# Optimization experiments

Measured on AMD Instinct MI355X. Metric: run time of the kernel, lower is better.

Reference implementation:

```python
import jax, jax.numpy as jnp
import numpy as np

EPS = 1e-4      # MovingBatchNorm eps
STEPS = 3       # fixed RK4 steps standing in for adaptive dopri5
B, N, D, C, H = 4, 2048, 3, 64, 512


def setup_inputs() -> dict:
    key = jax.random.key(0)
    ks = iter(jax.random.split(key, 40))
    f32 = jnp.float32

    def rn(shape, s=1.0):
        return jax.random.normal(next(ks), shape, dtype=f32) * s

    inp = {}
    inp['x'] = rn((B, N, D))
    inp['c'] = rn((B, N, C))
    for p in ('bn1', 'bn2'):
        inp[p + '_mean'] = rn((D,), 0.1)
        inp[p + '_var'] = jax.random.uniform(next(ks), (D,), dtype=f32, minval=0.5, maxval=1.5)
        inp[p + '_log_gamma'] = jnp.zeros((D,), f32)
        inp[p + '_beta'] = jnp.zeros((D,), f32)
    inp['sqrt_T'] = jnp.array([np.sqrt(0.5)], f32)  # train_T: T = sqrt_T**2
    dims = [(D, H), (H, H), (H, H), (H, D)]  # concatsquash (in, out)
    for i, (din, dout) in enumerate(dims):
        inp[f'W{i}'] = rn((dout, din), 0.05)
        inp[f'b{i}'] = jnp.zeros((dout,), f32)
        inp[f'Wg{i}'] = rn((dout, C + 1), 0.05)
        inp[f'bg{i}'] = jnp.zeros((dout,), f32)
        inp[f'Wb{i}'] = rn((dout, C + 1), 0.05)
    return inp


def _odenet(t, x, c, layers):
    # ConcatSquash MLP: lin(x)*sigmoid(hyper_gate([t,c])) + hyper_bias([t,c])
    ctx = jnp.concatenate([jnp.broadcast_to(t, c.shape[:-1] + (1,)).astype(x.dtype), c], axis=-1)
    h = x
    for i, (W, b, Wg, bg, Wb) in enumerate(layers):
        h = (h @ W.T + b) * jax.nn.sigmoid(ctx @ Wg.T + bg) + ctx @ Wb.T
        if i < len(layers) - 1:
            h = jnp.tanh(h)
    return h


def _aug_dyn(t, x, c, layers):
    # augmented CNF dynamics: (dx/dt, dlogp/dt) with exact divergence via D jvps
    f = lambda xx: _odenet(t, xx, c, layers)
    div = jnp.zeros(x.shape[:-1] + (1,), x.dtype)
    dx = None
    for i in range(x.shape[-1]):
        e = jnp.zeros_like(x).at[..., i].set(1.0)
        dx, jv = jax.jvp(f, (x,), (e,))
        div = div + jv[..., i:i + 1]
    return dx, -div


def _rk4(x0, lp0, c, layers, T):
    dt = T / STEPS

    def step(carry, i):
        x, lp = carry
        t = i.astype(x.dtype) * dt
        k1x, k1l = _aug_dyn(t, x, c, layers)
        k2x, k2l = _aug_dyn(t + 0.5 * dt, x + 0.5 * dt * k1x, c, layers)
        k3x, k3l = _aug_dyn(t + 0.5 * dt, x + 0.5 * dt * k2x, c, layers)
        k4x, k4l = _aug_dyn(t + dt, x + dt * k3x, c, layers)
        x = x + (dt / 6.0) * (k1x + 2.0 * k2x + 2.0 * k3x + k4x)
        lp = lp + (dt / 6.0) * (k1l + 2.0 * k2l + 2.0 * k3l + k4l)
        return (x, lp), None

    (x, lp), _ = jax.lax.scan(step, (x0, lp0), jnp.arange(STEPS))
    return x, lp


def _bn(x, lp, mean, var, log_gamma, beta):
    # MovingBatchNorm1d, eval mode; logdet = sum(log_gamma - 0.5*log(var+eps))
    y = (x - mean) * jnp.exp(log_gamma) / jnp.sqrt(var + EPS) + beta
    ld = jnp.sum(log_gamma - 0.5 * jnp.log(var + EPS))
    return y, lp - ld


def reference(x, c, bn1_mean, bn1_var, bn1_log_gamma, bn1_beta,
              bn2_mean, bn2_var, bn2_log_gamma, bn2_beta, sqrt_T,
              W0, b0, Wg0, bg0, Wb0, W1, b1, Wg1, bg1, Wb1,
              W2, b2, Wg2, bg2, Wb2, W3, b3, Wg3, bg3, Wb3):
    layers = [(W0, b0, Wg0, bg0, Wb0), (W1, b1, Wg1, bg1, Wb1),
              (W2, b2, Wg2, bg2, Wb2), (W3, b3, Wg3, bg3, Wb3)]
    lp = jnp.zeros(x.shape[:-1] + (1,), x.dtype)  # (B,N,1)
    x, lp = _bn(x, lp, bn1_mean, bn1_var, bn1_log_gamma, bn1_beta)
    T = sqrt_T[0] ** 2
    x, lp = _rk4(x, lp, c, layers, T)
    x, lp = _bn(x, lp, bn2_mean, bn2_var, bn2_log_gamma, bn2_beta)
    return x, jnp.sum(lp, axis=(1, 2))
```

## Files before the change

kernel.cpp:

```cpp
#include <hip/hip_runtime.h>
#include <hip/hip_fp8.h>

#define PTS 8192
#define HDIM 512
#define BN_EPS 1e-4f
#define HSTRB 528
#define TS 256.0f
#define SCL1 0x7f7f7f7f

typedef unsigned short u16;
typedef unsigned char u8;
typedef long long i64;
typedef u16 u16x8 __attribute__((ext_vector_type(8)));
typedef short s16x8 __attribute__((ext_vector_type(8)));
typedef float f32x4 __attribute__((ext_vector_type(4)));
typedef float f32x2 __attribute__((ext_vector_type(2)));
typedef int i32x4 __attribute__((ext_vector_type(4)));
typedef int i32x8 __attribute__((ext_vector_type(8)));

__device__ __forceinline__ float bf2f(u16 u) {
  unsigned x = ((unsigned)u) << 16;
  return __builtin_bit_cast(float, x);
}
__device__ __forceinline__ u16 f2bf(float f) {
  unsigned x = __builtin_bit_cast(unsigned, f);
  x += 0x7fffu + ((x >> 16) & 1u);
  return (u16)(x >> 16);
}
__device__ __forceinline__ u8 f2f8(float x) {
  int v = __builtin_amdgcn_cvt_pk_fp8_f32(x, x, 0, false);
  return (u8)(v & 0xff);
}
__device__ __forceinline__ unsigned pk4_f8(float a, float b, float c, float d) {
  int v = __builtin_amdgcn_cvt_pk_fp8_f32(a, b, 0, false);
  v = __builtin_amdgcn_cvt_pk_fp8_f32(c, d, v, true);
  return (unsigned)v;
}
__device__ __forceinline__ float sigf(float x) {
  return __builtin_amdgcn_rcpf(1.f + __expf(-x));
}
__device__ __forceinline__ float fast_tanh(float x) {
  float e = __expf(2.f * x);
  return 1.f - 2.f * __builtin_amdgcn_rcpf(e + 1.f);
}
__device__ __forceinline__ void gl2lds16(const u16* g, u16* l) {
  __builtin_amdgcn_global_load_lds(
      (const __attribute__((address_space(1))) void*)g,
      (__attribute__((address_space(3))) void*)l, 16, 0, 0);
}
__device__ __forceinline__ i32x8 ld32(const u8* p) {
  i32x4 lo = *(const i32x4*)p;
  i32x4 hi = *(const i32x4*)(p + 16);
  return __builtin_shufflevector(lo, hi, 0, 1, 2, 3, 4, 5, 6, 7);
}

#define MFMA_SC(A, B, C) \
  __builtin_amdgcn_mfma_scale_f32_16x16x128_f8f6f4((A), (B), (C), 0, 0, 0, SCL1, 0, SCL1)

#define MX_HALF(WL, HB, H)                                                  \
  {                                                                         \
    _Pragma("unroll")                                                       \
    for (int zi = 0; zi < 2; ++zi)                                          \
      _Pragma("unroll")                                                     \
      for (int zj = 0; zj < 2; ++zj)                                        \
        _Pragma("unroll")                                                   \
        for (int zr = 0; zr < 4; ++zr) acc[zi][zj][zr] = 0.f;               \
    const u8* wp = (WL) + (H) * 4096;                                       \
    _Pragma("unroll 1")                                                     \
    for (int c = 0; c < 4; ++c) {                                           \
      const u8* hc = (HB) + c * 128;                                        \
      i32x8 af0 = ld32(hc);                                                 \
      i32x8 af1 = ld32(hc + (size_t)16 * HSTRB);                            \
      i32x8 bA = ld32(wp);                                                  \
      i32x8 bB = ld32(wp + 2048);                                           \
      __builtin_amdgcn_sched_barrier(0);                                    \
      __builtin_amdgcn_s_setprio(1);                                        \
      acc[0][0] = MFMA_SC(af0, bA, acc[0][0]);                              \
      acc[1][0] = MFMA_SC(af1, bA, acc[1][0]);                              \
      acc[0][1] = MFMA_SC(af0, bB, acc[0][1]);                              \
      acc[1][1] = MFMA_SC(af1, bB, acc[1][1]);                              \
      __builtin_amdgcn_s_setprio(0);                                        \
      __builtin_amdgcn_sched_barrier(0);                                    \
      wp += 65536;                                                          \
    }                                                                       \
  }

#define EPI1_HALF(H)                                                        \
  {                                                                         \
    asm("" : "+v"(g1p));                                                    \
    unsigned g1v[2][2];                                                     \
    _Pragma("unroll")                                                       \
    for (int jl = 0; jl < 2; ++jl)                                          \
      _Pragma("unroll")                                                     \
      for (int i = 0; i < 2; ++i)                                           \
        g1v[jl][i] = *(const unsigned*)(g1p + (size_t)i * 4096 +            \
                                        ((H) * 2 + jl) * 32);               \
    _Pragma("unroll")                                                       \
    for (int jl = 0; jl < 2; ++jl) {                                        \
      int n = n0 + ((H) * 2 + jl) * 16 + lr;                                \
      f32x4 e1 = *(const f32x4*)(a.E1 + (size_t)n * 4);                     \
      _Pragma("unroll")                                                     \
      for (int i = 0; i < 2; ++i) {                                         \
        unsigned d = g1v[jl][i];                                            \
        float gate = sigf(bf2f((u16)(d & 0xffffu)) + t * e1[1]);            \
        float bias = bf2f((u16)(d >> 16)) + t * e1[2];                      \
        f32x4 u = acc[i][jl];                                               \
        float z = fmaf(u[0] + e1[0], gate, bias);                           \
        float hh = fast_tanh(z);                                            \
        float wmf = (1.f - hh * hh) * gate;                                 \
        int row = i * 16 + quad * 4;                                        \
        HsB[(size_t)row * HSTRB + n] = f2f8(hh);                            \
        HsB[(size_t)(row + 1) * HSTRB + n] = f2f8(u[1] * wmf);              \
        HsB[(size_t)(row + 2) * HSTRB + n] = f2f8(u[2] * wmf);              \
        HsB[(size_t)(row + 3) * HSTRB + n] = f2f8(u[3] * wmf);              \
      }                                                                     \
    }                                                                       \
  }

#define EPI2_HALF(H)                                                        \
  {                                                                         \
    asm("" : "+v"(g2p));                                                    \
    unsigned g2v[2][2];                                                     \
    _Pragma("unroll")                                                       \
    for (int jl = 0; jl < 2; ++jl)                                          \
      _Pragma("unroll")                                                     \
      for (int i = 0; i < 2; ++i)                                           \
        g2v[jl][i] = *(const unsigned*)(g2p + (size_t)i * 4096 +            \
                                        ((H) * 2 + jl) * 32);               \
    _Pragma("unroll")                                                       \
    for (int i = 0; i < 2; ++i) {                                           \
      float v0 = 0.f, v1 = 0.f, v2 = 0.f, v3 = 0.f, v4 = 0.f, v5 = 0.f;     \
      _Pragma("unroll")                                                     \
      for (int jl = 0; jl < 2; ++jl) {                                      \
        int n = n0 + ((H) * 2 + jl) * 16 + lr;                              \
        f32x4 ea = *(const f32x4*)(a.E2 + (size_t)n * 8);                   \
        f32x2 eb = *(const f32x2*)(a.E2 + (size_t)n * 8 + 4);               \
        unsigned d = g2v[jl][i];                                            \
        float gate = sigf(bf2f((u16)(d & 0xffffu)) + t * ea[1]);            \
        float bias = bf2f((u16)(d >> 16)) + t * ea[2];                      \
        f32x4 u = acc[i][jl];                                               \
        float z = fmaf(u[0] + ea[0], gate, bias);                           \
        float hh = fast_tanh(z);                                            \
        float wmf = (1.f - hh * hh) * gate;                                 \
        float w30 = ea[3], w31 = eb[0], w32 = eb[1];                        \
        v0 = fmaf(hh, w30, v0);                                             \
        v1 = fmaf(hh, w31, v1);                                             \
        v2 = fmaf(hh, w32, v2);                                             \
        v3 = fmaf(u[1] * wmf, w30, v3);                                     \
        v4 = fmaf(u[2] * wmf, w31, v4);                                     \
        v5 = fmaf(u[3] * wmf, w32, v5);                                     \
      }                                                                     \
      _Pragma("unroll")                                                     \
      for (int mask = 1; mask <= 8; mask <<= 1) {                           \
        v0 += __shfl_xor(v0, mask);                                         \
        v1 += __shfl_xor(v1, mask);                                         \
        v2 += __shfl_xor(v2, mask);                                         \
        v3 += __shfl_xor(v3, mask);                                         \
        v4 += __shfl_xor(v4, mask);                                         \
        v5 += __shfl_xor(v5, mask);                                         \
      }                                                                     \
      float val = (lr == 0) ? v0 : (lr == 1) ? v1 : (lr == 2) ? v2          \
                : (lr == 3) ? v3 * (1.f / TS) : (lr == 4) ? v4 * (1.f / TS) \
                : v5 * (1.f / TS);                                          \
      int pl = i * 4 + quad;                                                \
      if (lr < 6) {                                                         \
        if ((H) == 0) part[w][pl][lr] = val;                                \
        else part[w][pl][lr] += val;                                        \
      }                                                                     \
    }                                                                       \
  }

struct PrepArgs {
  const float *W1, *W2;
  u8 *W1s, *W2s;
  const float* c;
  u16* cb;
  const float *Wg0, *Wg1, *Wg2, *Wb0, *Wb1, *Wb2;
  const float *bg0, *bg1, *bg2;
  u16* Wpack;
  float* bias_pack;
  const float *x, *m1, *v1, *lg1, *be1;
  float *x_cur;
  const float *Wg3, *bg3, *Wb3;
  float *G3, *B3;
  const float *W0, *b0, *b1, *b2, *W3;
  float *E0, *E1, *E2;
};
__global__ void prep_kernel(PrepArgs a) {
  int i = blockIdx.x * 256 + threadIdx.x;
  if (i < 512 * 512) {
    int n = i >> 9, k = i & 511;
    int c = k >> 7, q2 = (k >> 5) & 3, b = k & 31;
    int w = n >> 6, j = (n >> 4) & 3, lr = n & 15;
    size_t d = (size_t)c * 65536 + (size_t)w * 8192 + (size_t)j * 2048 +
               (size_t)(q2 * 16 + lr) * 32 + b;
    a.W1s[d] = f2f8(a.W1[i]);
    a.W2s[d] = f2f8(a.W2[i]);
  }
  if (i < PTS * 64) a.cb[i] = f2bf(a.c[i]);
  if (i < 6 * 512 * 64) {
    int sec = i >> 15;
    int within = i & 32767;
    int o = within >> 6, k = within & 63;
    const float* src[6] = {a.Wg0, a.Wg1, a.Wg2, a.Wb0, a.Wb1, a.Wb2};
    a.Wpack[i] = f2bf(src[sec][o * 65 + 1 + k]);
  }
  if (i < 3072) {
    int sec = i >> 9, o = i & 511;
    const float* bgl[3] = {a.bg0, a.bg1, a.bg2};
    a.bias_pack[i] = (sec < 3) ? bgl[sec][o] : 0.f;
  }
  if (i < 512) {
    int o = i;
    a.E0[o * 8 + 0] = a.W0[o * 3];
    a.E0[o * 8 + 1] = a.W0[o * 3 + 1];
    a.E0[o * 8 + 2] = a.W0[o * 3 + 2];
    a.E0[o * 8 + 3] = a.b0[o];
    a.E0[o * 8 + 4] = a.Wg0[o * 65];
    a.E0[o * 8 + 5] = a.Wb0[o * 65];
    a.E0[o * 8 + 6] = 0.f; a.E0[o * 8 + 7] = 0.f;
    a.E1[o * 4 + 0] = a.b1[o];
    a.E1[o * 4 + 1] = a.Wg1[o * 65];
    a.E1[o * 4 + 2] = a.Wb1[o * 65];
    a.E1[o * 4 + 3] = 0.f;
    a.E2[o * 8 + 0] = a.b2[o];
    a.E2[o * 8 + 1] = a.Wg2[o * 65];
    a.E2[o * 8 + 2] = a.Wb2[o * 65];
    a.E2[o * 8 + 3] = a.W3[o];
    a.E2[o * 8 + 4] = a.W3[512 + o];
    a.E2[o * 8 + 5] = a.W3[1024 + o];
    a.E2[o * 8 + 6] = 0.f; a.E2[o * 8 + 7] = 0.f;
  }
  if (i < PTS * 3) {
    int d = i % 3;
    a.x_cur[i] = (a.x[i] - a.m1[d]) * __expf(a.lg1[d]) * rsqrtf(a.v1[d] + BN_EPS) + a.be1[d];
  }
  {
    int lane = threadIdx.x & 63;
    int p = (blockIdx.x * 256 + threadIdx.x) >> 6;
    float cv = a.c[(size_t)p * 64 + lane];
    float ag[3], ab[3];
    #pragma unroll
    for (int o = 0; o < 3; ++o) {
      ag[o] = cv * a.Wg3[o * 65 + 1 + lane];
      ab[o] = cv * a.Wb3[o * 65 + 1 + lane];
    }
    #pragma unroll
    for (int off = 32; off > 0; off >>= 1) {
      #pragma unroll
      for (int o = 0; o < 3; ++o) {
        ag[o] += __shfl_xor(ag[o], off);
        ab[o] += __shfl_xor(ab[o], off);
      }
    }
    if (lane == 0) {
      #pragma unroll
      for (int o = 0; o < 3; ++o) {
        a.G3[p * 3 + o] = ag[o] + a.bg3[o];
        a.B3[p * 3 + o] = ab[o];
      }
    }
  }
}

struct GatesGemmArgs {
  const u16 *A, *W;
  const float* bias;
  u16* GBi;
};
__global__ __launch_bounds__(256) void gates_gemm(GatesGemmArgs a) {
  __shared__ u16 As[128 * 32];
  __shared__ u16 Bs[128 * 32];
  int tid = threadIdx.x;
  int m0 = blockIdx.x * 128, n0 = blockIdx.y * 128;
  int wave = tid >> 6, lane = tid & 63;
  int wm = (wave & 1) * 64, wn = (wave >> 1) * 64;
  int lr = lane & 15, quad = lane >> 4;

  int rowS = tid >> 2, colS = (tid & 3) * 8;
  const u16* gA0 = a.A + (size_t)(m0 + rowS) * 64 + colS;
  const u16* gB0 = a.W + (size_t)(n0 + rowS) * 64 + colS;
  u16* sA0 = &As[tid * 8];
  u16* sA1 = &As[2048 + tid * 8];
  u16* sB0 = &Bs[tid * 8];
  u16* sB1 = &Bs[2048 + tid * 8];

  f32x4 acc[4][4];
  #pragma unroll
  for (int i = 0; i < 4; ++i)
    #pragma unroll
    for (int j = 0; j < 4; ++j)
      #pragma unroll
      for (int r = 0; r < 4; ++r) acc[i][j][r] = 0.f;

  for (int k0 = 0; k0 < 64; k0 += 32) {
    if (k0) __syncthreads();
    gl2lds16(gA0 + k0, sA0);
    gl2lds16(gA0 + (size_t)64 * 64 + k0, sA1);
    gl2lds16(gB0 + k0, sB0);
    gl2lds16(gB0 + (size_t)64 * 64 + k0, sB1);
    __syncthreads();
    s16x8 af[4], bfr[4];
    #pragma unroll
    for (int i = 0; i < 4; ++i)
      af[i] = *(const s16x8*)&As[(wm + i * 16 + lr) * 32 + quad * 8];
    #pragma unroll
    for (int j = 0; j < 4; ++j)
      bfr[j] = *(const s16x8*)&Bs[(wn + j * 16 + lr) * 32 + quad * 8];
    #pragma unroll
    for (int i = 0; i < 4; ++i)
      #pragma unroll
      for (int j = 0; j < 4; ++j)
        acc[i][j] = __builtin_amdgcn_mfma_f32_16x16x32_bf16(af[i], bfr[j], acc[i][j], 0, 0, 0);
  }

  #pragma unroll
  for (int j = 0; j < 4; ++j) {
    int n = n0 + wn + j * 16 + lr;
    int sec = n >> 9, col = n & 511;
    int l = (sec < 3) ? sec : sec - 3;
    int off = col * 2 + ((sec < 3) ? 0 : 1);
    float bv = a.bias[n];
    u16* outp = a.GBi + (size_t)l * PTS * 1024 + off;
    #pragma unroll
    for (int i = 0; i < 4; ++i) {
      int mrow = m0 + wm + i * 16 + quad * 4;
      #pragma unroll
      for (int r = 0; r < 4; ++r)
        outp[(size_t)(mrow + r) * 1024] = f2bf(acc[i][j][r] + bv);
    }
  }
}

struct FlowArgs {
  const float* sqrtT;
  const float *G3, *B3, *Wg3, *Wb3, *b3;
  const float* x0;
  const u16 *GBi0, *GBi1, *GBi2;
  const float *E0, *E1, *E2;
  const u8 *W1s, *W2s;
  const float *m2, *v2, *lg2, *be2;
  float* out_x;
  float* lp_state;
};

__global__ __launch_bounds__(512, 6) void flow_kernel(FlowArgs a) {
  __shared__ __align__(16) u8 HsA[32 * HSTRB];
  __shared__ __align__(16) u8 HsB[32 * HSTRB];
  __shared__ float part[8][8][8];
  __shared__ float xs[2][8][3], kxs[8][3];
  __shared__ float kls[8], lps[8];
  __shared__ float g3s[8][3], b3s[8][3];

  int tid = threadIdx.x;
  int w = tid >> 6, lane = tid & 63, lr = lane & 15, quad = lane >> 4;
  int n0 = w * 64;
  int p0 = blockIdx.x * 8;
  int pl0 = tid >> 6;
  int base_o = (tid & 63) * 8;
  bool desig = (tid & 63) == 0;
  float s0 = a.sqrtT[0];
  float dt = s0 * s0 * (1.f / 3.f);

  const u8* w1l = a.W1s + (size_t)w * 8192 + (size_t)lane * 32;
  const u8* w2l = a.W2s + (size_t)w * 8192 + (size_t)lane * 32;
  const u8* hbA = (const u8*)HsA + (size_t)lr * HSTRB + quad * 32;
  const u8* hbB = (const u8*)HsB + (size_t)lr * HSTRB + quad * 32;

  float wg3r[3], wb3r[3], b3r[3];
  #pragma unroll
  for (int r = 0; r < 3; ++r) {
    wg3r[r] = a.Wg3[r * 65];
    wb3r[r] = a.Wb3[r * 65];
    b3r[r] = a.b3[r];
  }

  const u16* g0p = a.GBi0 + (size_t)(p0 + pl0) * 1024 + 2 * base_o;
  const u16* g1p = a.GBi1 + (size_t)(p0 + quad) * 1024 + 2 * (n0 + lr);
  const u16* g2p = a.GBi2 + (size_t)(p0 + quad) * 1024 + 2 * (n0 + lr);

  if (desig) {
    #pragma unroll
    for (int r = 0; r < 3; ++r) {
      xs[0][pl0][r] = a.x0[(p0 + pl0) * 3 + r];
      g3s[pl0][r] = a.G3[(p0 + pl0) * 3 + r];
      b3s[pl0][r] = a.B3[(p0 + pl0) * 3 + r];
    }
    lps[pl0] = 0.f;
  }
  u16x8 gc0 = *(const u16x8*)(g0p);
  u16x8 gc1 = *(const u16x8*)(g0p + 8);
  __syncthreads();

  #pragma unroll 1
  for (int s = 0; s < 12; ++s) {
    int sub = s & 3;
    float t = ((float)(s >> 2) + ((sub == 0) ? 0.f : (sub == 3) ? 1.f : 0.5f)) * dt;

    float o0, o1, o2;
    if (s == 0) {
      o0 = xs[0][pl0][0]; o1 = xs[0][pl0][1]; o2 = xs[0][pl0][2];
    } else {
      int m = (s - 1) & 3, q = (s - 1) >> 2;
      float tp = ((float)q + ((m == 0) ? 0.f : (m == 3) ? 1.f : 0.5f)) * dt;
      float fr0 = 0.f, fr1 = 0.f, fr2 = 0.f, fr3 = 0.f, fr4 = 0.f, fr5 = 0.f;
      #pragma unroll
      for (int ww = 0; ww < 8; ++ww) {
        f32x4 pa = *(const f32x4*)&part[ww][pl0][0];
        f32x2 pb = *(const f32x2*)&part[ww][pl0][4];
        fr0 += pa[0]; fr1 += pa[1]; fr2 += pa[2];
        fr3 += pa[3]; fr4 += pb[0]; fr5 += pb[1];
      }
      float ga0 = sigf(g3s[pl0][0] + tp * wg3r[0]);
      float ga1 = sigf(g3s[pl0][1] + tp * wg3r[1]);
      float ga2 = sigf(g3s[pl0][2] + tp * wg3r[2]);
      float dx0 = fmaf(fr0 + b3r[0], ga0, b3s[pl0][0] + tp * wb3r[0]);
      float dx1 = fmaf(fr1 + b3r[1], ga1, b3s[pl0][1] + tp * wb3r[1]);
      float dx2 = fmaf(fr2 + b3r[2], ga2, b3s[pl0][2] + tp * wb3r[2]);
      float klv = -(fr3 * ga0 + fr4 * ga1 + fr5 * ga2);
      float bx0 = xs[q & 1][pl0][0];
      float bx1 = xs[q & 1][pl0][1];
      float bx2 = xs[q & 1][pl0][2];
      if (m == 3) {
        float sc = dt * (1.f / 6.f);
        o0 = bx0 + sc * (kxs[pl0][0] + dx0);
        o1 = bx1 + sc * (kxs[pl0][1] + dx1);
        o2 = bx2 + sc * (kxs[pl0][2] + dx2);
        if (desig) {
          xs[(q + 1) & 1][pl0][0] = o0;
          xs[(q + 1) & 1][pl0][1] = o1;
          xs[(q + 1) & 1][pl0][2] = o2;
          lps[pl0] += sc * (kls[pl0] + klv);
        }
      } else {
        float cf = (m == 2) ? dt : 0.5f * dt;
        o0 = fmaf(cf, dx0, bx0);
        o1 = fmaf(cf, dx1, bx1);
        o2 = fmaf(cf, dx2, bx2);
        if (desig) {
          if (m == 0) {
            kxs[pl0][0] = dx0; kxs[pl0][1] = dx1; kxs[pl0][2] = dx2;
            kls[pl0] = klv;
          } else {
            kxs[pl0][0] += 2.f * dx0; kxs[pl0][1] += 2.f * dx1; kxs[pl0][2] += 2.f * dx2;
            kls[pl0] += 2.f * klv;
          }
        }
      }
    }

    {
      u16x8 gcv[2] = {gc0, gc1};
      #pragma unroll
      for (int cc = 0; cc < 2; ++cc) {
        u16x8 v = gcv[cc];
        float hk[4], d0k[4], d1k[4], d2k[4];
        #pragma unroll
        for (int k = 0; k < 4; ++k) {
          int o = base_o + cc * 4 + k;
          f32x4 e = *(const f32x4*)(a.E0 + (size_t)o * 8);
          f32x2 e2 = *(const f32x2*)(a.E0 + (size_t)o * 8 + 4);
          float u = fmaf(e[0], o0, fmaf(e[1], o1, e[2] * o2)) + e[3];
          float gate = sigf(bf2f(v[2 * k]) + t * e2[0]);
          float bias = bf2f(v[2 * k + 1]) + t * e2[1];
          float z = fmaf(u, gate, bias);
          float h = fast_tanh(z);
          float wm = (1.f - h * h) * gate * TS;
          hk[k] = h;
          d0k[k] = wm * e[0];
          d1k[k] = wm * e[1];
          d2k[k] = wm * e[2];
        }
        size_t hbb = (size_t)(pl0 * 4) * HSTRB + base_o + cc * 4;
        *(unsigned*)(HsA + hbb) = pk4_f8(hk[0], hk[1], hk[2], hk[3]);
        *(unsigned*)(HsA + hbb + HSTRB) = pk4_f8(d0k[0], d0k[1], d0k[2], d0k[3]);
        *(unsigned*)(HsA + hbb + 2 * HSTRB) = pk4_f8(d1k[0], d1k[1], d1k[2], d1k[3]);
        *(unsigned*)(HsA + hbb + 3 * HSTRB) = pk4_f8(d2k[0], d2k[1], d2k[2], d2k[3]);
      }
    }
    __syncthreads();

    f32x4 acc[2][2];
    MX_HALF(w1l, hbA, 0)
    EPI1_HALF(0)
    MX_HALF(w1l, hbA, 1)
    EPI1_HALF(1)
    __syncthreads();

    MX_HALF(w2l, hbB, 0)
    EPI2_HALF(0)
    MX_HALF(w2l, hbB, 1)
    asm("" : "+v"(g0p));
    gc0 = *(const u16x8*)(g0p);
    gc1 = *(const u16x8*)(g0p + 8);
    EPI2_HALF(1)
    __syncthreads();
  }

  if (desig) {
    int p = p0 + pl0;
    float tp = 3.f * dt;
    float fr0 = 0.f, fr1 = 0.f, fr2 = 0.f, fr3 = 0.f, fr4 = 0.f, fr5 = 0.f;
    #pragma unroll
    for (int ww = 0; ww < 8; ++ww) {
      f32x4 pa = *(const f32x4*)&part[ww][pl0][0];
      f32x2 pb = *(const f32x2*)&part[ww][pl0][4];
      fr0 += pa[0]; fr1 += pa[1]; fr2 += pa[2];
      fr3 += pa[3]; fr4 += pb[0]; fr5 += pb[1];
    }
    float ga0 = sigf(g3s[pl0][0] + tp * wg3r[0]);
    float ga1 = sigf(g3s[pl0][1] + tp * wg3r[1]);
    float ga2 = sigf(g3s[pl0][2] + tp * wg3r[2]);
    float dx[3];
    dx[0] = fmaf(fr0 + b3r[0], ga0, b3s[pl0][0] + tp * wb3r[0]);
    dx[1] = fmaf(fr1 + b3r[1], ga1, b3s[pl0][1] + tp * wb3r[1]);
    dx[2] = fmaf(fr2 + b3r[2], ga2, b3s[pl0][2] + tp * wb3r[2]);
    float klv = -(fr3 * ga0 + fr4 * ga1 + fr5 * ga2);
    float sc = dt * (1.f / 6.f);
    #pragma unroll
    for (int r = 0; r < 3; ++r) {
      float xf = xs[0][pl0][r] + sc * (kxs[pl0][r] + dx[r]);
      a.out_x[p * 3 + r] =
          (xf - a.m2[r]) * __expf(a.lg2[r]) * rsqrtf(a.v2[r] + BN_EPS) + a.be2[r];
    }
    a.lp_state[p] = lps[pl0] + sc * (kls[pl0] + klv);
  }
}

__global__ void finish_lp(const float* __restrict__ lp_state,
                          const float* __restrict__ v1, const float* __restrict__ lg1,
                          const float* __restrict__ v2, const float* __restrict__ lg2,
                          float* __restrict__ out) {
  int b = blockIdx.x, tid = threadIdx.x;
  float s = 0.f;
  for (int n = tid; n < 2048; n += 256) s += lp_state[b * 2048 + n];
  __shared__ float red[256];
  red[tid] = s;
  __syncthreads();
  for (int w = 128; w > 0; w >>= 1) {
    if (tid < w) red[tid] += red[tid + w];
    __syncthreads();
  }
  if (tid == 0) {
    float ld = 0.f;
    for (int d = 0; d < 3; ++d) {
      ld += lg1[d] - 0.5f * logf(v1[d] + BN_EPS);
      ld += lg2[d] - 0.5f * logf(v2[d] + BN_EPS);
    }
    out[b] = red[0] - 2048.f * ld;
  }
}

extern "C" void kernel_launch(void* const* d_in, const int* in_sizes, int n_in,
                              void* d_out, int out_size, void* d_ws, size_t ws_size,
                              hipStream_t stream) {
  const float* x        = (const float*)d_in[0];
  const float* c        = (const float*)d_in[1];
  const float* bn1_mean = (const float*)d_in[2];
  const float* bn1_var  = (const float*)d_in[3];
  const float* bn1_lg   = (const float*)d_in[4];
  const float* bn1_beta = (const float*)d_in[5];
  const float* bn2_mean = (const float*)d_in[6];
  const float* bn2_var  = (const float*)d_in[7];
  const float* bn2_lg   = (const float*)d_in[8];
  const float* bn2_beta = (const float*)d_in[9];
  const float* sqrtT    = (const float*)d_in[10];
  const float* W0  = (const float*)d_in[11];
  const float* b0  = (const float*)d_in[12];
  const float* Wg0 = (const float*)d_in[13];
  const float* bg0 = (const float*)d_in[14];
  const float* Wb0 = (const float*)d_in[15];
  const float* W1  = (const float*)d_in[16];
  const float* b1  = (const float*)d_in[17];
  const float* Wg1 = (const float*)d_in[18];
  const float* bg1 = (const float*)d_in[19];
  const float* Wb1 = (const float*)d_in[20];
  const float* W2  = (const float*)d_in[21];
  const float* b2  = (const float*)d_in[22];
  const float* Wg2 = (const float*)d_in[23];
  const float* bg2 = (const float*)d_in[24];
  const float* Wb2 = (const float*)d_in[25];
  const float* W3  = (const float*)d_in[26];
  const float* b3  = (const float*)d_in[27];
  const float* Wg3 = (const float*)d_in[28];
  const float* bg3 = (const float*)d_in[29];
  const float* Wb3 = (const float*)d_in[30];

  char* base = (char*)d_ws;
  size_t off = 0;
  auto alloc = [&](size_t bytes) -> void* {
    void* pp = base + off;
    off += (bytes + 255) & ~(size_t)255;
    return pp;
  };
  u8* W1s = (u8*)alloc((size_t)512 * 512);
  u8* W2s = (u8*)alloc((size_t)512 * 512);
  u16* cb  = (u16*)alloc((size_t)PTS * 64 * 2);
  u16* Wpack = (u16*)alloc((size_t)6 * 512 * 64 * 2);
  float* bias_pack = (float*)alloc((size_t)3072 * 4);
  u16* GBi = (u16*)alloc((size_t)3 * PTS * 1024 * 2);
  const size_t SZi = (size_t)PTS * 1024;
  u16* GBi0 = GBi;
  u16* GBi1 = GBi + SZi;
  u16* GBi2 = GBi + 2 * SZi;
  float* G3f = (float*)alloc((size_t)PTS * 3 * 4);
  float* B3f = (float*)alloc((size_t)PTS * 3 * 4);
  float* E0 = (float*)alloc((size_t)512 * 8 * 4);
  float* E1 = (float*)alloc((size_t)512 * 4 * 4);
  float* E2 = (float*)alloc((size_t)512 * 8 * 4);
  float* x_cur    = (float*)alloc((size_t)PTS * 3 * 4);
  float* lp_state = (float*)alloc((size_t)PTS * 4);
  (void)ws_size; (void)in_sizes; (void)n_in; (void)out_size;

  PrepArgs pa{W1, W2, W1s, W2s, c, cb, Wg0, Wg1, Wg2, Wb0, Wb1, Wb2,
              bg0, bg1, bg2, Wpack, bias_pack, x, bn1_mean, bn1_var,
              bn1_lg, bn1_beta, x_cur, Wg3, bg3, Wb3, G3f, B3f,
              W0, b0, b1, b2, W3, E0, E1, E2};
  prep_kernel<<<2048, 256, 0, stream>>>(pa);

  GatesGemmArgs gg{cb, Wpack, bias_pack, GBi};
  gates_gemm<<<dim3(64, 24), 256, 0, stream>>>(gg);

  FlowArgs fa{sqrtT, G3f, B3f, Wg3, Wb3, b3, x_cur, GBi0, GBi1, GBi2,
              E0, E1, E2, W1s, W2s, bn2_mean, bn2_var, bn2_lg, bn2_beta,
              (float*)d_out, lp_state};
  flow_kernel<<<PTS / 8, 512, 0, stream>>>(fa);

  finish_lp<<<4, 256, 0, stream>>>(lp_state, bn1_var, bn1_lg, bn2_var, bn2_lg,
                                   (float*)d_out + PTS * 3);
}
```

Before: 643.2 us.

## Process two point groups per block and interleave their layer pipelines

Each block now handles 16 points split into two 8-point halves with double-buffered activation tiles. The MFMA work of one half overlaps the epilogue and layer-0 work of the other. Each wave's GEMM tile widens to 4 column groups, so each A fragment load feeds twice as many MFMAs. This halves the grid and cuts per-block weight re-reads and barriers per point. The cost is higher register and LDS pressure and a more complex schedule.

After: 726.7 us. 1.13x slower.

```diff
diff --git a/kernel.cpp b/kernel.cpp
--- a/kernel.cpp
+++ b/kernel.cpp
@@ -57,117 +57,217 @@
 #define MFMA_SC(A, B, C) \
   __builtin_amdgcn_mfma_scale_f32_16x16x128_f8f6f4((A), (B), (C), 0, 0, 0, SCL1, 0, SCL1)
 
-#define MX_HALF(WL, HB, H)                                                  \
+#define MXCHUNK(ACC, WP, HC)                                                \
+    {                                                                       \
+      i32x8 af0 = ld32(HC);                                                 \
+      i32x8 af1 = ld32((HC) + (size_t)16 * HSTRB);                          \
+      i32x8 bA = ld32(WP);                                                  \
+      i32x8 bB = ld32((WP) + 2048);                                         \
+      __builtin_amdgcn_sched_barrier(0);                                    \
+      __builtin_amdgcn_s_setprio(1);                                        \
+      ACC[0][0] = MFMA_SC(af0, bA, ACC[0][0]);                              \
+      ACC[1][0] = MFMA_SC(af1, bA, ACC[1][0]);                              \
+      ACC[0][1] = MFMA_SC(af0, bB, ACC[0][1]);                              \
+      ACC[1][1] = MFMA_SC(af1, bB, ACC[1][1]);                              \
+      __builtin_amdgcn_s_setprio(0);                                        \
+      __builtin_amdgcn_sched_barrier(0);                                    \
+      bA = ld32((WP) + 4096);                                               \
+      bB = ld32((WP) + 6144);                                               \
+      __builtin_amdgcn_sched_barrier(0);                                    \
+      __builtin_amdgcn_s_setprio(1);                                        \
+      ACC[0][2] = MFMA_SC(af0, bA, ACC[0][2]);                              \
+      ACC[1][2] = MFMA_SC(af1, bA, ACC[1][2]);                              \
+      ACC[0][3] = MFMA_SC(af0, bB, ACC[0][3]);                              \
+      ACC[1][3] = MFMA_SC(af1, bB, ACC[1][3]);                              \
+      __builtin_amdgcn_s_setprio(0);                                        \
+      __builtin_amdgcn_sched_barrier(0);                                    \
+    }
+
+#define MXG(ACC, WL, HB, PREFETCH)                                          \
   {                                                                         \
     _Pragma("unroll")                                                       \
     for (int zi = 0; zi < 2; ++zi)                                          \
       _Pragma("unroll")                                                     \
-      for (int zj = 0; zj < 2; ++zj)                                        \
+      for (int zj = 0; zj < 4; ++zj)                                        \
         _Pragma("unroll")                                                   \
-        for (int zr = 0; zr < 4; ++zr) acc[zi][zj][zr] = 0.f;               \
-    const u8* wp = (WL) + (H) * 4096;                                       \
+        for (int zr = 0; zr < 4; ++zr) ACC[zi][zj][zr] = 0.f;               \
+    const u8* wp = (WL);                                                    \
     _Pragma("unroll 1")                                                     \
-    for (int c = 0; c < 4; ++c) {                                           \
+    for (int c = 0; c < 3; ++c) {                                           \
       const u8* hc = (HB) + c * 128;                                        \
-      i32x8 af0 = ld32(hc);                                                 \
-      i32x8 af1 = ld32(hc + (size_t)16 * HSTRB);                            \
-      i32x8 bA = ld32(wp);                                                  \
-      i32x8 bB = ld32(wp + 2048);                                           \
-      __builtin_amdgcn_sched_barrier(0);                                    \
-      __builtin_amdgcn_s_setprio(1);                                        \
-      acc[0][0] = MFMA_SC(af0, bA, acc[0][0]);                              \
-      acc[1][0] = MFMA_SC(af1, bA, acc[1][0]);                              \
-      acc[0][1] = MFMA_SC(af0, bB, acc[0][1]);                              \
-      acc[1][1] = MFMA_SC(af1, bB, acc[1][1]);                              \
-      __builtin_amdgcn_s_setprio(0);                                        \
-      __builtin_amdgcn_sched_barrier(0);                                    \
+      MXCHUNK(ACC, wp, hc)                                                  \
       wp += 65536;                                                          \
     }                                                                       \
-  }
-
-#define EPI1_HALF(H)                                                        \
+    PREFETCH                                                                \
+    {                                                                       \
+      const u8* hc = (HB) + 3 * 128;                                        \
+      MXCHUNK(ACC, wp, hc)                                                  \
+    }                                                                       \
+  }
+
+#define FOLDM(HH, SS)                                                       \
   {                                                                         \
-    asm("" : "+v"(g1p));                                                    \
-    unsigned g1v[2][2];                                                     \
+    int ptg = (HH) * 8 + ptl;                                               \
+    if ((SS) == 0) {                                                        \
+      o0 = xs[0][ptg][0]; o1 = xs[0][ptg][1]; o2 = xs[0][ptg][2];           \
+    } else {                                                                \
+      int m = ((SS) - 1) & 3, q = ((SS) - 1) >> 2;                          \
+      float tp = ((float)q + ((m == 0) ? 0.f : (m == 3) ? 1.f : 0.5f)) * dt;\
+      float fr0 = 0.f, fr1 = 0.f, fr2 = 0.f, fr3 = 0.f, fr4 = 0.f, fr5 = 0.f;\
+      _Pragma("unroll")                                                     \
+      for (int ww = 0; ww < 8; ++ww) {                                      \
+        f32x4 pa = *(const f32x4*)&part[ww][ptg][0];                        \
+        f32x2 pb = *(const f32x2*)&part[ww][ptg][4];                        \
+        fr0 += pa[0]; fr1 += pa[1]; fr2 += pa[2];                           \
+        fr3 += pa[3]; fr4 += pb[0]; fr5 += pb[1];                           \
+      }                                                                     \
+      float ga0 = sigf(g3s[ptg][0] + tp * a.Wg3[0]);                        \
+      float ga1 = sigf(g3s[ptg][1] + tp * a.Wg3[65]);                       \
+      float ga2 = sigf(g3s[ptg][2] + tp * a.Wg3[130]);                      \
+      float dx0 = fmaf(fr0 + a.b3[0], ga0, b3s[ptg][0] + tp * a.Wb3[0]);    \
+      float dx1 = fmaf(fr1 + a.b3[1], ga1, b3s[ptg][1] + tp * a.Wb3[65]);   \
+      float dx2 = fmaf(fr2 + a.b3[2], ga2, b3s[ptg][2] + tp * a.Wb3[130]);  \
+      float klv = -(fr3 * ga0 + fr4 * ga1 + fr5 * ga2);                     \
+      float bx0 = xs[q & 1][ptg][0];                                        \
+      float bx1 = xs[q & 1][ptg][1];                                        \
+      float bx2 = xs[q & 1][ptg][2];                                        \
+      if (m == 3) {                                                         \
+        float sc = dt * (1.f / 6.f);                                        \
+        o0 = bx0 + sc * (kxs[ptg][0] + dx0);                                \
+        o1 = bx1 + sc * (kxs[ptg][1] + dx1);                                \
+        o2 = bx2 + sc * (kxs[ptg][2] + dx2);                                \
+        if (desig) {                                                        \
+          xs[(q + 1) & 1][ptg][0] = o0;                                     \
+          xs[(q + 1) & 1][ptg][1] = o1;                                     \
+          xs[(q + 1) & 1][ptg][2] = o2;                                     \
+          lps[ptg] += sc * (kls[ptg] + klv);                                \
+        }                                                                   \
+      } else {                                                              \
+        float cf = (m == 2) ? dt : 0.5f * dt;                               \
+        o0 = fmaf(cf, dx0, bx0);                                            \
+        o1 = fmaf(cf, dx1, bx1);                                            \
+        o2 = fmaf(cf, dx2, bx2);                                            \
+        if (desig) {                                                        \
+          if (m == 0) {                                                     \
+            kxs[ptg][0] = dx0; kxs[ptg][1] = dx1; kxs[ptg][2] = dx2;        \
+            kls[ptg] = klv;                                                 \
+          } else {                                                          \
+            kxs[ptg][0] += 2.f * dx0; kxs[ptg][1] += 2.f * dx1;             \
+            kxs[ptg][2] += 2.f * dx2;                                       \
+            kls[ptg] += 2.f * klv;                                          \
+          }                                                                 \
+        }                                                                   \
+      }                                                                     \
+    }                                                                       \
+  }
+
+#define L0M(HD, TT)                                                         \
+  {                                                                         \
     _Pragma("unroll")                                                       \
-    for (int jl = 0; jl < 2; ++jl)                                          \
+    for (int cc = 0; cc < 2; ++cc) {                                        \
+      u16x8 v = cc ? gcB : gcA;                                             \
+      float hk[4], d0k[4], d1k[4], d2k[4];                                  \
+      _Pragma("unroll")                                                     \
+      for (int k = 0; k < 4; ++k) {                                         \
+        int o = colb + cc * 4 + k;                                          \
+        f32x4 e = *(const f32x4*)(a.E0 + (size_t)o * 8);                    \
+        f32x2 e2 = *(const f32x2*)(a.E0 + (size_t)o * 8 + 4);               \
+        float u = fmaf(e[0], o0, fmaf(e[1], o1, e[2] * o2)) + e[3];         \
+        float gate = sigf(bf2f(v[2 * k]) + (TT) * e2[0]);                   \
+        float bias = bf2f(v[2 * k + 1]) + (TT) * e2[1];                     \
+        float z = fmaf(u, gate, bias);                                      \
+        float hh = fast_tanh(z);                                            \
+        float wm = (1.f - hh * hh) * gate * TS;                             \
+        hk[k] = hh;                                                         \
+        d0k[k] = wm * e[0];                                                 \
+        d1k[k] = wm * e[1];                                                 \
+        d2k[k] = wm * e[2];                                                 \
+      }                                                                     \
+      size_t hbb = (size_t)(ptl * 4) * HSTRB + colb + cc * 4;               \
+      *(unsigned*)((HD) + hbb) = pk4_f8(hk[0], hk[1], hk[2], hk[3]);        \
+      *(unsigned*)((HD) + hbb + HSTRB) = pk4_f8(d0k[0], d0k[1], d0k[2], d0k[3]); \
+      *(unsigned*)((HD) + hbb + 2 * HSTRB) = pk4_f8(d1k[0], d1k[1], d1k[2], d1k[3]); \
+      *(unsigned*)((HD) + hbb + 3 * HSTRB) = pk4_f8(d2k[0], d2k[1], d2k[2], d2k[3]); \
+    }                                                                       \
+  }
+
+#define EPI1M(ACC, HD)                                                      \
+  _Pragma("unroll")                                                         \
+  for (int j = 0; j < 4; ++j) {                                             \
+    int n = n0 + j * 16 + lr;                                               \
+    f32x4 e1 = *(const f32x4*)(a.E1 + (size_t)n * 4);                       \
+    _Pragma("unroll")                                                       \
+    for (int i = 0; i < 2; ++i) {                                           \
+      unsigned d = gv[j][i];                                                \
+      float gate = sigf(bf2f((u16)(d & 0xffffu)) + t * e1[1]);              \
+      float bias = bf2f((u16)(d >> 16)) + t * e1[2];                        \
+      f32x4 u = ACC[i][j];                                                  \
+      float z = fmaf(u[0] + e1[0], gate, bias);                             \
+      float hh = fast_tanh(z);                                              \
+      float wmf = (1.f - hh * hh) * gate;                                   \
+      int row = i * 16 + quad * 4;                                          \
+      (HD)[(size_t)row * HSTRB + n] = f2f8(hh);                             \
+      (HD)[(size_t)(row + 1) * HSTRB + n] = f2f8(u[1] * wmf);               \
+      (HD)[(size_t)(row + 2) * HSTRB + n] = f2f8(u[2] * wmf);               \
+      (HD)[(size_t)(row + 3) * HSTRB + n] = f2f8(u[3] * wmf);               \
+    }                                                                       \
+  }
+
+#define EPI2M(ACC, HH)                                                      \
+  _Pragma("unroll")                                                         \
+  for (int i = 0; i < 2; ++i) {                                             \
+    float v0 = 0.f, v1 = 0.f, v2 = 0.f, v3 = 0.f, v4 = 0.f, v5 = 0.f;       \
+    _Pragma("unroll")                                                       \
+    for (int j = 0; j < 4; ++j) {                                           \
+      int n = n0 + j * 16 + lr;                                             \
+      f32x4 ea = *(const f32x4*)(a.E2 + (size_t)n * 8);                     \
+      f32x2 eb = *(const f32x2*)(a.E2 + (size_t)n * 8 + 4);                 \
+      unsigned d = gv[j][i];                                                \
+      float gate = sigf(bf2f((u16)(d & 0xffffu)) + t * ea[1]);              \
+      float bias = bf2f((u16)(d >> 16)) + t * ea[2];                        \
+      f32x4 u = ACC[i][j];                                                  \
+      float z = fmaf(u[0] + ea[0], gate, bias);                             \
+      float hh = fast_tanh(z);                                              \
+      float wmf = (1.f - hh * hh) * gate;                                   \
+      float w30 = ea[3], w31 = eb[0], w32 = eb[1];                          \
+      v0 = fmaf(hh, w30, v0);                                               \
+      v1 = fmaf(hh, w31, v1);                                               \
+      v2 = fmaf(hh, w32, v2);                                               \
+      v3 = fmaf(u[1] * wmf, w30, v3);                                       \
+      v4 = fmaf(u[2] * wmf, w31, v4);                                       \
+      v5 = fmaf(u[3] * wmf, w32, v5);                                       \
+    }                                                                       \
+    _Pragma("unroll")                                                       \
+    for (int mask = 1; mask <= 8; mask <<= 1) {                             \
+      v0 += __shfl_xor(v0, mask);                                           \
+      v1 += __shfl_xor(v1, mask);                                           \
+      v2 += __shfl_xor(v2, mask);                                           \
+      v3 += __shfl_xor(v3, mask);                                           \
+      v4 += __shfl_xor(v4, mask);                                           \
+      v5 += __shfl_xor(v5, mask);                                           \
+    }                                                                       \
+    float val = (lr == 0) ? v0 : (lr == 1) ? v1 : (lr == 2) ? v2            \
+              : (lr == 3) ? v3 * (1.f / TS) : (lr == 4) ? v4 * (1.f / TS)   \
+              : v5 * (1.f / TS);                                            \
+    if (lr < 6) part[w][(HH) * 8 + i * 4 + quad][lr] = val;                 \
+  }
+
+#define GLD(BP, HH)                                                         \
+  {                                                                         \
+    const u16* gp_ = (BP); asm("" : "+v"(gp_));                             \
+    _Pragma("unroll")                                                       \
+    for (int j = 0; j < 4; ++j)                                             \
       _Pragma("unroll")                                                     \
       for (int i = 0; i < 2; ++i)                                           \
-        g1v[jl][i] = *(const unsigned*)(g1p + (size_t)i * 4096 +            \
-                                        ((H) * 2 + jl) * 32);               \
-    _Pragma("unroll")                                                       \
-    for (int jl = 0; jl < 2; ++jl) {                                        \
-      int n = n0 + ((H) * 2 + jl) * 16 + lr;                                \
-      f32x4 e1 = *(const f32x4*)(a.E1 + (size_t)n * 4);                     \
-      _Pragma("unroll")                                                     \
-      for (int i = 0; i < 2; ++i) {                                         \
-        unsigned d = g1v[jl][i];                                            \
-        float gate = sigf(bf2f((u16)(d & 0xffffu)) + t * e1[1]);            \
-        float bias = bf2f((u16)(d >> 16)) + t * e1[2];                      \
-        f32x4 u = acc[i][jl];                                               \
-        float z = fmaf(u[0] + e1[0], gate, bias);                           \
-        float hh = fast_tanh(z);                                            \
-        float wmf = (1.f - hh * hh) * gate;                                 \
-        int row = i * 16 + quad * 4;                                        \
-        HsB[(size_t)row * HSTRB + n] = f2f8(hh);                            \
-        HsB[(size_t)(row + 1) * HSTRB + n] = f2f8(u[1] * wmf);              \
-        HsB[(size_t)(row + 2) * HSTRB + n] = f2f8(u[2] * wmf);              \
-        HsB[(size_t)(row + 3) * HSTRB + n] = f2f8(u[3] * wmf);              \
-      }                                                                     \
-    }                                                                       \
-  }
-
-#define EPI2_HALF(H)                                                        \
+        gv[j][i] = *(const unsigned*)(gp_ + (HH) * 8192 +                   \
+                                      (size_t)i * 4096 + j * 32);           \
+  }
+
+#define GCLD(HH)                                                            \
   {                                                                         \
-    asm("" : "+v"(g2p));                                                    \
-    unsigned g2v[2][2];                                                     \
-    _Pragma("unroll")                                                       \
-    for (int jl = 0; jl < 2; ++jl)                                          \
-      _Pragma("unroll")                                                     \
-      for (int i = 0; i < 2; ++i)                                           \
-        g2v[jl][i] = *(const unsigned*)(g2p + (size_t)i * 4096 +            \
-                                        ((H) * 2 + jl) * 32);               \
-    _Pragma("unroll")                                                       \
-    for (int i = 0; i < 2; ++i) {                                           \
-      float v0 = 0.f, v1 = 0.f, v2 = 0.f, v3 = 0.f, v4 = 0.f, v5 = 0.f;     \
-      _Pragma("unroll")                                                     \
-      for (int jl = 0; jl < 2; ++jl) {                                      \
-        int n = n0 + ((H) * 2 + jl) * 16 + lr;                              \
-        f32x4 ea = *(const f32x4*)(a.E2 + (size_t)n * 8);                   \
-        f32x2 eb = *(const f32x2*)(a.E2 + (size_t)n * 8 + 4);               \
-        unsigned d = g2v[jl][i];                                            \
-        float gate = sigf(bf2f((u16)(d & 0xffffu)) + t * ea[1]);            \
-        float bias = bf2f((u16)(d >> 16)) + t * ea[2];                      \
-        f32x4 u = acc[i][jl];                                               \
-        float z = fmaf(u[0] + ea[0], gate, bias);                           \
-        float hh = fast_tanh(z);                                            \
-        float wmf = (1.f - hh * hh) * gate;                                 \
-        float w30 = ea[3], w31 = eb[0], w32 = eb[1];                        \
-        v0 = fmaf(hh, w30, v0);                                             \
-        v1 = fmaf(hh, w31, v1);                                             \
-        v2 = fmaf(hh, w32, v2);                                             \
-        v3 = fmaf(u[1] * wmf, w30, v3);                                     \
-        v4 = fmaf(u[2] * wmf, w31, v4);                                     \
-        v5 = fmaf(u[3] * wmf, w32, v5);                                     \
-      }                                                                     \
-      _Pragma("unroll")                                                     \
-      for (int mask = 1; mask <= 8; mask <<= 1) {                           \
-        v0 += __shfl_xor(v0, mask);                                         \
-        v1 += __shfl_xor(v1, mask);                                         \
-        v2 += __shfl_xor(v2, mask);                                         \
-        v3 += __shfl_xor(v3, mask);                                         \
-        v4 += __shfl_xor(v4, mask);                                         \
-        v5 += __shfl_xor(v5, mask);                                         \
-      }                                                                     \
-      float val = (lr == 0) ? v0 : (lr == 1) ? v1 : (lr == 2) ? v2          \
-                : (lr == 3) ? v3 * (1.f / TS) : (lr == 4) ? v4 * (1.f / TS) \
-                : v5 * (1.f / TS);                                          \
-      int pl = i * 4 + quad;                                                \
-      if (lr < 6) {                                                         \
-        if ((H) == 0) part[w][pl][lr] = val;                                \
-        else part[w][pl][lr] += val;                                        \
-      }                                                                     \
-    }                                                                       \
+    const u16* gp_ = g0p + (HH) * 8192; asm("" : "+v"(gp_));                \
+    gcA = *(const u16x8*)(gp_);                                             \
+    gcB = *(const u16x8*)(gp_ + 8);                                         \
   }
 
 struct PrepArgs {
@@ -344,186 +444,120 @@
   float* lp_state;
 };
 
-__global__ __launch_bounds__(512, 6) void flow_kernel(FlowArgs a) {
-  __shared__ __align__(16) u8 HsA[32 * HSTRB];
-  __shared__ __align__(16) u8 HsB[32 * HSTRB];
-  __shared__ float part[8][8][8];
-  __shared__ float xs[2][8][3], kxs[8][3];
-  __shared__ float kls[8], lps[8];
-  __shared__ float g3s[8][3], b3s[8][3];
+__global__ __launch_bounds__(512, 4) void flow_kernel(FlowArgs a) {
+  __shared__ __align__(16) u8 HA0[32 * HSTRB];
+  __shared__ __align__(16) u8 HA1[32 * HSTRB];
+  __shared__ __align__(16) u8 HB0[32 * HSTRB];
+  __shared__ __align__(16) u8 HB1[32 * HSTRB];
+  __shared__ float part[8][16][8];
+  __shared__ float xs[2][16][3], kxs[16][3];
+  __shared__ float kls[16], lps[16];
+  __shared__ float g3s[16][3], b3s[16][3];
 
   int tid = threadIdx.x;
   int w = tid >> 6, lane = tid & 63, lr = lane & 15, quad = lane >> 4;
   int n0 = w * 64;
-  int p0 = blockIdx.x * 8;
-  int pl0 = tid >> 6;
-  int base_o = (tid & 63) * 8;
+  int p0 = blockIdx.x * 16;
+  int ptl = tid >> 6;
+  int colb = (tid & 63) * 8;
   bool desig = (tid & 63) == 0;
   float s0 = a.sqrtT[0];
   float dt = s0 * s0 * (1.f / 3.f);
 
   const u8* w1l = a.W1s + (size_t)w * 8192 + (size_t)lane * 32;
   const u8* w2l = a.W2s + (size_t)w * 8192 + (size_t)lane * 32;
-  const u8* hbA = (const u8*)HsA + (size_t)lr * HSTRB + quad * 32;
-  const u8* hbB = (const u8*)HsB + (size_t)lr * HSTRB + quad * 32;
-
-  float wg3r[3], wb3r[3], b3r[3];
-  #pragma unroll
-  for (int r = 0; r < 3; ++r) {
-    wg3r[r] = a.Wg3[r * 65];
-    wb3r[r] = a.Wb3[r * 65];
-    b3r[r] = a.b3[r];
-  }
-
-  const u16* g0p = a.GBi0 + (size_t)(p0 + pl0) * 1024 + 2 * base_o;
+  const u8* hA0 = (const u8*)HA0 + (size_t)lr * HSTRB + quad * 32;
+  const u8* hA1 = (const u8*)HA1 + (size_t)lr * HSTRB + quad * 32;
+  const u8* hB0 = (const u8*)HB0 + (size_t)lr * HSTRB + quad * 32;
+  const u8* hB1 = (const u8*)HB1 + (size_t)lr * HSTRB + quad * 32;
+
+  const u16* g0p = a.GBi0 + (size_t)(p0 + ptl) * 1024 + 2 * colb;
   const u16* g1p = a.GBi1 + (size_t)(p0 + quad) * 1024 + 2 * (n0 + lr);
   const u16* g2p = a.GBi2 + (size_t)(p0 + quad) * 1024 + 2 * (n0 + lr);
 
-  if (desig) {
+  if (tid < 16) {
+    int p = p0 + tid;
     #pragma unroll
     for (int r = 0; r < 3; ++r) {
-      xs[0][pl0][r] = a.x0[(p0 + pl0) * 3 + r];
-      g3s[pl0][r] = a.G3[(p0 + pl0) * 3 + r];
-      b3s[pl0][r] = a.B3[(p0 + pl0) * 3 + r];
-    }
-    lps[pl0] = 0.f;
-  }
-  u16x8 gc0 = *(const u16x8*)(g0p);
-  u16x8 gc1 = *(const u16x8*)(g0p + 8);
+      xs[0][tid][r] = a.x0[p * 3 + r];
+      g3s[tid][r] = a.G3[p * 3 + r];
+      b3s[tid][r] = a.B3[p * 3 + r];
+    }
+    lps[tid] = 0.f;
+  }
+
+  u16x8 gcA, gcB;
+  unsigned gv[4][2];
+  float o0, o1, o2;
+
+  GCLD(0)
   __syncthreads();
+  FOLDM(0, 0)
+  L0M(HA0, 0.f)
+  __syncthreads();
+
+  f32x4 accA[2][4], accB[2][4];
 
   #pragma unroll 1
   for (int s = 0; s < 12; ++s) {
     int sub = s & 3;
     float t = ((float)(s >> 2) + ((sub == 0) ? 0.f : (sub == 3) ? 1.f : 0.5f)) * dt;
 
-    float o0, o1, o2;
-    if (s == 0) {
-      o0 = xs[0][pl0][0]; o1 = xs[0][pl0][1]; o2 = xs[0][pl0][2];
-    } else {
-      int m = (s - 1) & 3, q = (s - 1) >> 2;
-      float tp = ((float)q + ((m == 0) ? 0.f : (m == 3) ? 1.f : 0.5f)) * dt;
-      float fr0 = 0.f, fr1 = 0.f, fr2 = 0.f, fr3 = 0.f, fr4 = 0.f, fr5 = 0.f;
-      #pragma unroll
-      for (int ww = 0; ww < 8; ++ww) {
-        f32x4 pa = *(const f32x4*)&part[ww][pl0][0];
-        f32x2 pb = *(const f32x2*)&part[ww][pl0][4];
-        fr0 += pa[0]; fr1 += pa[1]; fr2 += pa[2];
-        fr3 += pa[3]; fr4 += pb[0]; fr5 += pb[1];
-      }
-      float ga0 = sigf(g3s[pl0][0] + tp * wg3r[0]);
-      float ga1 = sigf(g3s[pl0][1] + tp * wg3r[1]);
-      float ga2 = sigf(g3s[pl0][2] + tp * wg3r[2]);
-      float dx0 = fmaf(fr0 + b3r[0], ga0, b3s[pl0][0] + tp * wb3r[0]);
-      float dx1 = fmaf(fr1 + b3r[1], ga1, b3s[pl0][1] + tp * wb3r[1]);
-      float dx2 = fmaf(fr2 + b3r[2], ga2, b3s[pl0][2] + tp * wb3r[2]);
-      float klv = -(fr3 * ga0 + fr4 * ga1 + fr5 * ga2);
-      float bx0 = xs[q & 1][pl0][0];
-      float bx1 = xs[q & 1][pl0][1];
-      float bx2 = xs[q & 1][pl0][2];
-      if (m == 3) {
-        float sc = dt * (1.f / 6.f);
-        o0 = bx0 + sc * (kxs[pl0][0] + dx0);
-        o1 = bx1 + sc * (kxs[pl0][1] + dx1);
-        o2 = bx2 + sc * (kxs[pl0][2] + dx2);
-        if (desig) {
-          xs[(q + 1) & 1][pl0][0] = o0;
-          xs[(q + 1) & 1][pl0][1] = o1;
-          xs[(q + 1) & 1][pl0][2] = o2;
-          lps[pl0] += sc * (kls[pl0] + klv);
-        }
-      } else {
-        float cf = (m == 2) ? dt : 0.5f * dt;
-        o0 = fmaf(cf, dx0, bx0);
-        o1 = fmaf(cf, dx1, bx1);
-        o2 = fmaf(cf, dx2, bx2);
-        if (desig) {
-          if (m == 0) {
-            kxs[pl0][0] = dx0; kxs[pl0][1] = dx1; kxs[pl0][2] = dx2;
-            kls[pl0] = klv;
-          } else {
-            kxs[pl0][0] += 2.f * dx0; kxs[pl0][1] += 2.f * dx1; kxs[pl0][2] += 2.f * dx2;
-            kls[pl0] += 2.f * klv;
-          }
-        }
-      }
-    }
-
-    {
-      u16x8 gcv[2] = {gc0, gc1};
-      #pragma unroll
-      for (int cc = 0; cc < 2; ++cc) {
-        u16x8 v = gcv[cc];
-        float hk[4], d0k[4], d1k[4], d2k[4];
-        #pragma unroll
-        for (int k = 0; k < 4; ++k) {
-          int o = base_o + cc * 4 + k;
-          f32x4 e = *(const f32x4*)(a.E0 + (size_t)o * 8);
-          f32x2 e2 = *(const f32x2*)(a.E0 + (size_t)o * 8 + 4);
-          float u = fmaf(e[0], o0, fmaf(e[1], o1, e[2] * o2)) + e[3];
-          float gate = sigf(bf2f(v[2 * k]) + t * e2[0]);
-          float bias = bf2f(v[2 * k + 1]) + t * e2[1];
-          float z = fmaf(u, gate, bias);
-          float h = fast_tanh(z);
-          float wm = (1.f - h * h) * gate * TS;
-          hk[k] = h;
-          d0k[k] = wm * e[0];
-          d1k[k] = wm * e[1];
-          d2k[k] = wm * e[2];
-        }
-        size_t hbb = (size_t)(pl0 * 4) * HSTRB + base_o + cc * 4;
-        *(unsigned*)(HsA + hbb) = pk4_f8(hk[0], hk[1], hk[2], hk[3]);
-        *(unsigned*)(HsA + hbb + HSTRB) = pk4_f8(d0k[0], d0k[1], d0k[2], d0k[3]);
-        *(unsigned*)(HsA + hbb + 2 * HSTRB) = pk4_f8(d1k[0], d1k[1], d1k[2], d1k[3]);
-        *(unsigned*)(HsA + hbb + 3 * HSTRB) = pk4_f8(d2k[0], d2k[1], d2k[2], d2k[3]);
-      }
-    }
+    MXG(accA, w1l, hA0, GCLD(1))
+    FOLDM(1, s)
+    L0M(HA1, t)
     __syncthreads();
 
-    f32x4 acc[2][2];
-    MX_HALF(w1l, hbA, 0)
-    EPI1_HALF(0)
-    MX_HALF(w1l, hbA, 1)
-    EPI1_HALF(1)
+    MXG(accB, w1l, hA1, GLD(g1p, 0))
+    EPI1M(accA, HB0)
     __syncthreads();
 
-    MX_HALF(w2l, hbB, 0)
-    EPI2_HALF(0)
-    MX_HALF(w2l, hbB, 1)
-    asm("" : "+v"(g0p));
-    gc0 = *(const u16x8*)(g0p);
-    gc1 = *(const u16x8*)(g0p + 8);
-    EPI2_HALF(1)
+    MXG(accA, w2l, hB0, GLD(g1p, 1))
+    EPI1M(accB, HB1)
     __syncthreads();
-  }
-
-  if (desig) {
-    int p = p0 + pl0;
+
+    MXG(accB, w2l, hB1, GLD(g2p, 0) GCLD(0))
+    EPI2M(accA, 0)
+    __syncthreads();
+
+    GLD(g2p, 1)
+    EPI2M(accB, 1)
+    if (s < 11) {
+      int sn = s + 1, sb = sn & 3;
+      float tn = ((float)(sn >> 2) + ((sb == 0) ? 0.f : (sb == 3) ? 1.f : 0.5f)) * dt;
+      FOLDM(0, sn)
+      L0M(HA0, tn)
+    }
+    __syncthreads();
+  }
+
+  if (tid < 16) {
+    int p = p0 + tid;
     float tp = 3.f * dt;
     float fr0 = 0.f, fr1 = 0.f, fr2 = 0.f, fr3 = 0.f, fr4 = 0.f, fr5 = 0.f;
     #pragma unroll
     for (int ww = 0; ww < 8; ++ww) {
-      f32x4 pa = *(const f32x4*)&part[ww][pl0][0];
-      f32x2 pb = *(const f32x2*)&part[ww][pl0][4];
+      f32x4 pa = *(const f32x4*)&part[ww][tid][0];
+      f32x2 pb = *(const f32x2*)&part[ww][tid][4];
       fr0 += pa[0]; fr1 += pa[1]; fr2 += pa[2];
       fr3 += pa[3]; fr4 += pb[0]; fr5 += pb[1];
     }
-    float ga0 = sigf(g3s[pl0][0] + tp * wg3r[0]);
-    float ga1 = sigf(g3s[pl0][1] + tp * wg3r[1]);
-    float ga2 = sigf(g3s[pl0][2] + tp * wg3r[2]);
+    float ga0 = sigf(g3s[tid][0] + tp * a.Wg3[0]);
+    float ga1 = sigf(g3s[tid][1] + tp * a.Wg3[65]);
+    float ga2 = sigf(g3s[tid][2] + tp * a.Wg3[130]);
     float dx[3];
-    dx[0] = fmaf(fr0 + b3r[0], ga0, b3s[pl0][0] + tp * wb3r[0]);
-    dx[1] = fmaf(fr1 + b3r[1], ga1, b3s[pl0][1] + tp * wb3r[1]);
-    dx[2] = fmaf(fr2 + b3r[2], ga2, b3s[pl0][2] + tp * wb3r[2]);
+    dx[0] = fmaf(fr0 + a.b3[0], ga0, b3s[tid][0] + tp * a.Wb3[0]);
+    dx[1] = fmaf(fr1 + a.b3[1], ga1, b3s[tid][1] + tp * a.Wb3[65]);
+    dx[2] = fmaf(fr2 + a.b3[2], ga2, b3s[tid][2] + tp * a.Wb3[130]);
     float klv = -(fr3 * ga0 + fr4 * ga1 + fr5 * ga2);
     float sc = dt * (1.f / 6.f);
     #pragma unroll
     for (int r = 0; r < 3; ++r) {
-      float xf = xs[0][pl0][r] + sc * (kxs[pl0][r] + dx[r]);
+      float xf = xs[0][tid][r] + sc * (kxs[tid][r] + dx[r]);
       a.out_x[p * 3 + r] =
           (xf - a.m2[r]) * __expf(a.lg2[r]) * rsqrtf(a.v2[r] + BN_EPS) + a.be2[r];
     }
-    a.lp_state[p] = lps[pl0] + sc * (kls[pl0] + klv);
+    a.lp_state[p] = lps[tid] + sc * (kls[tid] + klv);
   }
 }
 
@@ -624,7 +658,7 @@
   FlowArgs fa{sqrtT, G3f, B3f, Wg3, Wb3, b3, x_cur, GBi0, GBi1, GBi2,
               E0, E1, E2, W1s, W2s, bn2_mean, bn2_var, bn2_lg, bn2_beta,
               (float*)d_out, lp_state};
-  flow_kernel<<<PTS / 8, 512, 0, stream>>>(fa);
+  flow_kernel<<<PTS / 16, 512, 0, stream>>>(fa);
 
   finish_lp<<<4, 256, 0, stream>>>(lp_state, bn1_var, bn1_lg, bn2_var, bn2_lg,
                                    (float*)d_out + PTS * 3);
```
